# Optimization experiments

Hardware: AMD Instinct MI355X
Metric: run time of the kernel (lower is better)

## Reference

```python
import jax, jax.numpy as jnp
import numpy as np

H, DI, N, K, R, FF = 2048, 4096, 16, 4, 128, 5632
B, S = 2, 1024
EPS = 1e-6


def rmsnorm(x, w):
    v = jnp.mean(x * x, axis=-1, keepdims=True)
    return x * jax.lax.rsqrt(v + EPS) * w


def setup_inputs() -> dict:
    key = jax.random.key(0)
    ks = jax.random.split(key, 16)
    sc = 0.02
    inp = {
        "hidden_states": jax.random.normal(ks[0], (B, S, H), jnp.float32),
        "input_ln_w": jnp.ones((H,), jnp.float32),
        "w_in": jax.random.normal(ks[1], (2 * DI, H), jnp.float32) * sc,
        "conv_w": jax.random.normal(ks[2], (DI, 1, K), jnp.float32) * 0.3,
        "conv_b": jax.random.normal(ks[3], (DI,), jnp.float32) * sc,
        "w_x": jax.random.normal(ks[4], (R + 2 * N, DI), jnp.float32) * sc,
        "dt_ln_w": jnp.ones((R,), jnp.float32),
        "b_ln_w": jnp.ones((N,), jnp.float32),
        "c_ln_w": jnp.ones((N,), jnp.float32),
        "w_dt": jax.random.normal(ks[5], (DI, R), jnp.float32) * sc,
        "b_dt": jax.random.normal(ks[6], (DI,), jnp.float32) * sc - 4.0,
        "A_log": jnp.broadcast_to(jnp.log(jnp.arange(1, N + 1, dtype=jnp.float32)), (DI, N)),
        "D_skip": jnp.ones((DI,), jnp.float32),
        "w_out": jax.random.normal(ks[7], (H, DI), jnp.float32) * sc,
        "pre_ff_ln_w": jnp.ones((H,), jnp.float32),
        "w_gate": jax.random.normal(ks[8], (FF, H), jnp.float32) * sc,
        "w_up": jax.random.normal(ks[9], (FF, H), jnp.float32) * sc,
        "w_down": jax.random.normal(ks[10], (H, FF), jnp.float32) * sc,
    }
    return inp


def causal_conv1d(x, w, b):
    # x: [B,S,DI], w: [DI,1,K] depthwise, left-pad K-1 (causal)
    y = jax.lax.conv_general_dilated(
        x.transpose(0, 2, 1), w,
        window_strides=(1,), padding=[(K - 1, 0)],
        dimension_numbers=("NCH", "OIH", "NCH"),
        feature_group_count=DI)
    return (y + b[None, :, None]).transpose(0, 2, 1)


def selective_scan(u, A, Bm, Cm, Dp, dt):
    # u,dt: [B,S,DI]; A: [DI,N]; Bm,Cm: [B,S,N]
    def step(h, xs):
        dt_t, B_t, C_t, u_t = xs  # [B,DI],[B,N],[B,N],[B,DI]
        dA = jnp.exp(dt_t[:, :, None] * A)                      # [B,DI,N]
        dBu = dt_t[:, :, None] * B_t[:, None, :] * u_t[:, :, None]
        h = dA * h + dBu
        y = jnp.einsum("bdn,bn->bd", h, C_t)
        return h, y

    xs = (dt.transpose(1, 0, 2), Bm.transpose(1, 0, 2),
          Cm.transpose(1, 0, 2), u.transpose(1, 0, 2))
    h0 = jnp.zeros((u.shape[0], DI, N), u.dtype)
    _, ys = jax.lax.scan(step, h0, xs)
    return ys.transpose(1, 0, 2) + u * Dp  # [B,S,DI]


def reference(hidden_states, input_ln_w, w_in, conv_w, conv_b, w_x, dt_ln_w,
              b_ln_w, c_ln_w, w_dt, b_dt, A_log, D_skip, w_out, pre_ff_ln_w,
              w_gate, w_up, w_down):
    residual = hidden_states
    x = rmsnorm(hidden_states, input_ln_w)

    # --- Mamba mixer ---
    proj = x @ w_in.T                       # [B,S,2*DI]
    u, gate = jnp.split(proj, 2, axis=-1)
    u = jax.nn.silu(causal_conv1d(u, conv_w, conv_b))
    ssm_p = u @ w_x.T                       # [B,S,R+2N]
    t_r, Bm, Cm = jnp.split(ssm_p, [R, R + N], axis=-1)
    t_r = rmsnorm(t_r, dt_ln_w)
    Bm = rmsnorm(Bm, b_ln_w)
    Cm = rmsnorm(Cm, c_ln_w)
    dt = jax.nn.softplus(t_r @ w_dt.T + b_dt)  # [B,S,DI]
    A = -jnp.exp(A_log)
    y = selective_scan(u, A, Bm, Cm, D_skip, dt)
    y = y * jax.nn.silu(gate)
    mixer_out = y @ w_out.T                  # [B,S,H]

    hidden = residual + mixer_out
    residual = hidden
    h = rmsnorm(hidden, pre_ff_ln_w)
    ff = (jax.nn.silu(h @ w_gate.T) * (h @ w_up.T)) @ w_down.T
    return residual + ff
```

## Files before the change

### kernel.cpp

```cpp
#include <hip/hip_runtime.h>
#include <stdint.h>

#define H_   2048
#define DI_  4096
#define N_   16
#define K_   4
#define R_   128
#define FF_  5632
#define B_   2
#define S_   1024
#define MROWS (B_*S_)
#define PCH  16
#define CSTEPS (S_/PCH)

typedef float f32x4 __attribute__((ext_vector_type(4)));
typedef float f32x2 __attribute__((ext_vector_type(2)));
typedef __bf16 bf16x8 __attribute__((ext_vector_type(8)));

__device__ __forceinline__ unsigned short f2bf(float f) {
    union { float f; unsigned u; } v; v.f = f;
    unsigned r = v.u + 0x7fffu + ((v.u >> 16) & 1u);
    return (unsigned short)(r >> 16);
}

__device__ __forceinline__ float softplusf(float v) {
    return (v > 20.f) ? v : log1pf(__expf(v));
}

__device__ __forceinline__ void gload16(const void* g, void* lds) {
    __builtin_amdgcn_global_load_lds(
        (const __attribute__((address_space(1))) unsigned int*)(uintptr_t)g,
        (__attribute__((address_space(3))) unsigned int*)(unsigned int)(uintptr_t)lds,
        16, 0, 0);
}

__global__ __launch_bounds__(256, 2)
void gemm_bt(const unsigned short* __restrict__ A, const unsigned short* __restrict__ Bt,
             float* __restrict__ C, int M, int N, int K, int Kc)
{
    __shared__ __align__(16) unsigned short As[128 * 64];
    __shared__ __align__(16) unsigned short Bs[128 * 64];
    const int t = threadIdx.x;
    const int l = t & 63;
    const int wv = t >> 6;

    int nwg = gridDim.x * gridDim.y;
    int wg = blockIdx.y * gridDim.x + blockIdx.x;
    if ((nwg & 7) == 0) {
        int q = nwg >> 3;
        wg = (wg & 7) * q + (wg >> 3);
    }
    const int bx = wg % gridDim.x;
    const int by = wg / gridDim.x;
    const long m0 = (long)by * 128;
    const long n0 = (long)bx * 128;
    const int wm = (wv >> 1) * 64;
    const int wn = (wv & 1) * 64;
    const long kstart = (long)blockIdx.z * Kc;
    C += (long)blockIdx.z * M * (long)N;

    f32x4 acc[4][4] = {};

    const int tr = t >> 3;
    const int cs = (t & 7) ^ (tr & 7);
    const unsigned short* gA = A + (m0 + tr) * (long)K + kstart + cs * 8;
    const unsigned short* gB = Bt + (n0 + tr) * (long)K + kstart + cs * 8;
    const unsigned ldsbase = (unsigned)(t & 192) * 16;

    for (int kt = 0; kt < Kc; kt += 64) {
#pragma unroll
        for (int j = 0; j < 4; ++j) {
            gload16(gA + (long)j * 32 * K, (char*)As + j * 4096 + ldsbase);
            gload16(gB + (long)j * 32 * K, (char*)Bs + j * 4096 + ldsbase);
        }
        gA += 64; gB += 64;
        __syncthreads();
#pragma unroll
        for (int k0 = 0; k0 < 2; ++k0) {
            bf16x8 af[4], bfr[4];
#pragma unroll
            for (int i = 0; i < 4; ++i) {
                int rowa = wm + i * 16 + (l & 15);
                int ca = (k0 * 4 + (l >> 4)) ^ (rowa & 7);
                af[i] = *(const bf16x8*)(As + rowa * 64 + ca * 8);
                int rowb = wn + i * 16 + (l & 15);
                int cb = (k0 * 4 + (l >> 4)) ^ (rowb & 7);
                bfr[i] = *(const bf16x8*)(Bs + rowb * 64 + cb * 8);
            }
#pragma unroll
            for (int i = 0; i < 4; ++i)
#pragma unroll
                for (int jn = 0; jn < 4; ++jn)
                    acc[i][jn] = __builtin_amdgcn_mfma_f32_16x16x32_bf16(
                        af[i], bfr[jn], acc[i][jn], 0, 0, 0);
        }
        __syncthreads();
    }

    const int crow = (l >> 4) * 4;
    const int ccol = l & 15;
#pragma unroll
    for (int i = 0; i < 4; ++i) {
#pragma unroll
        for (int jn = 0; jn < 4; ++jn) {
            long row = m0 + wm + i * 16 + crow;
            long col = n0 + wn + jn * 16 + ccol;
            float* cp = C + row * (long)N + col;
#pragma unroll
            for (int q = 0; q < 4; ++q) cp[(long)q * N] = acc[i][jn][q];
        }
    }
}

__global__ __launch_bounds__(512, 1)
void gemm_bt256(const unsigned short* __restrict__ A, const unsigned short* __restrict__ Bt,
                float* __restrict__ C, int M, int N, int K, int Kc)
{
    __shared__ __align__(16) unsigned short As[2][256 * 64];
    __shared__ __align__(16) unsigned short Bs[2][256 * 64];
    const int t = threadIdx.x;
    const int l = t & 63;
    const int wv = t >> 6;
    const int wm = wv >> 2;
    const int wn = wv & 3;

    int nwg = gridDim.x * gridDim.y;
    int wg = blockIdx.y * gridDim.x + blockIdx.x;
    if ((nwg & 7) == 0) {
        int q = nwg >> 3;
        wg = (wg & 7) * q + (wg >> 3);
    }
    const int bx = wg % gridDim.x;
    const int by = wg / gridDim.x;
    const long m0 = (long)by * 256;
    const long n0 = (long)bx * 256;
    const long kstart = (long)blockIdx.z * Kc;
    C += (long)blockIdx.z * M * (long)N;

    f32x4 acc[8][4] = {};

    const int cs = (t & 7) ^ ((t >> 3) & 7);
    const unsigned short* gA = A + (m0 + (t >> 3)) * (long)K + kstart + cs * 8;
    const unsigned short* gB = Bt + (n0 + (t >> 3)) * (long)K + kstart + cs * 8;
    const int NT = Kc >> 6;

#pragma unroll
    for (int i = 0; i < 4; ++i)
        gload16(gA + (long)i * 64 * K, &As[0][t * 8 + i * 4096]);
#pragma unroll
    for (int i = 0; i < 4; ++i)
        gload16(gB + (long)i * 64 * K, &Bs[0][t * 8 + i * 4096]);

    for (int kt = 0; kt < NT; ++kt) {
        const int buf = kt & 1;
        const long koff = (long)((kt + 1 < NT) ? (kt + 1) : kt) * 64;
#pragma unroll
        for (int i = 0; i < 4; ++i)
            gload16(gA + koff + (long)i * 64 * K, &As[buf ^ 1][t * 8 + i * 4096]);
        asm volatile("s_waitcnt vmcnt(4)" ::: "memory");
        __builtin_amdgcn_sched_barrier(0);
        __builtin_amdgcn_s_barrier();
        __builtin_amdgcn_sched_barrier(0);
        {
            bf16x8 af[8], bfr[4];
#pragma unroll
            for (int nf = 0; nf < 4; ++nf) {
                int rowb = wn * 64 + nf * 16 + (l & 15);
                int cb = (l >> 4) ^ (rowb & 7);
                bfr[nf] = *(const bf16x8*)(&Bs[buf][rowb * 64 + cb * 8]);
            }
#pragma unroll
            for (int mf = 0; mf < 8; ++mf) {
                int rowa = wm * 128 + mf * 16 + (l & 15);
                int ca = (l >> 4) ^ (rowa & 7);
                af[mf] = *(const bf16x8*)(&As[buf][rowa * 64 + ca * 8]);
            }
            __builtin_amdgcn_s_setprio(1);
#pragma unroll
            for (int mf = 0; mf < 8; ++mf)
#pragma unroll
                for (int nf = 0; nf < 4; ++nf)
                    acc[mf][nf] = __builtin_amdgcn_mfma_f32_16x16x32_bf16(
                        af[mf], bfr[nf], acc[mf][nf], 0, 0, 0);
            __builtin_amdgcn_s_setprio(0);
        }
        __builtin_amdgcn_sched_barrier(0);
#pragma unroll
        for (int i = 0; i < 4; ++i)
            gload16(gB + koff + (long)i * 64 * K, &Bs[buf ^ 1][t * 8 + i * 4096]);
        {
            bf16x8 af[8], bfr[4];
#pragma unroll
            for (int nf = 0; nf < 4; ++nf) {
                int rowb = wn * 64 + nf * 16 + (l & 15);
                int cb = (4 + (l >> 4)) ^ (rowb & 7);
                bfr[nf] = *(const bf16x8*)(&Bs[buf][rowb * 64 + cb * 8]);
            }
#pragma unroll
            for (int mf = 0; mf < 8; ++mf) {
                int rowa = wm * 128 + mf * 16 + (l & 15);
                int ca = (4 + (l >> 4)) ^ (rowa & 7);
                af[mf] = *(const bf16x8*)(&As[buf][rowa * 64 + ca * 8]);
            }
            __builtin_amdgcn_s_setprio(1);
#pragma unroll
            for (int mf = 0; mf < 8; ++mf)
#pragma unroll
                for (int nf = 0; nf < 4; ++nf)
                    acc[mf][nf] = __builtin_amdgcn_mfma_f32_16x16x32_bf16(
                        af[mf], bfr[nf], acc[mf][nf], 0, 0, 0);
            __builtin_amdgcn_s_setprio(0);
        }
        __builtin_amdgcn_sched_barrier(0);
        __builtin_amdgcn_s_barrier();
        __builtin_amdgcn_sched_barrier(0);
    }

    const int crow = (l >> 4) * 4;
    const int ccol = l & 15;
#pragma unroll
    for (int mf = 0; mf < 8; ++mf) {
#pragma unroll
        for (int nf = 0; nf < 4; ++nf) {
            long row = m0 + wm * 128 + mf * 16 + crow;
            long col = n0 + wn * 64 + nf * 16 + ccol;
            float* cp = C + row * (long)N + col;
#pragma unroll
            for (int q = 0; q < 4; ++q) cp[(long)q * N] = acc[mf][nf][q];
        }
    }
}

__global__ __launch_bounds__(256)
void cvt_bf16(const float* __restrict__ x, unsigned short* __restrict__ y, long n)
{
    long i = ((long)blockIdx.x * 256 + threadIdx.x) * 4;
    if (i >= n) return;
    float4 v = *(const float4*)(x + i);
    ushort4 o;
    o.x = f2bf(v.x); o.y = f2bf(v.y); o.z = f2bf(v.z); o.w = f2bf(v.w);
    *(ushort4*)(y + i) = o;
}

__global__ __launch_bounds__(256)
void cvt_pad_wx(const float* __restrict__ x, unsigned short* __restrict__ y)
{
    long i = ((long)blockIdx.x * 256 + threadIdx.x) * 4;
    int row = (int)(i >> 12);
    ushort4 o;
    if (row < 160) {
        float4 v = *(const float4*)(x + i);
        o.x = f2bf(v.x); o.y = f2bf(v.y); o.z = f2bf(v.z); o.w = f2bf(v.w);
    } else { o.x = 0; o.y = 0; o.z = 0; o.w = 0; }
    *(ushort4*)(y + i) = o;
}

__global__ __launch_bounds__(256)
void rmsnorm_cast(const float* __restrict__ x, const float* __restrict__ w,
                  unsigned short* __restrict__ out)
{
    const long row = blockIdx.x;
    const float* xr = x + row * H_ + threadIdx.x * 8;
    float4 v0 = *(const float4*)xr;
    float4 v1 = *(const float4*)(xr + 4);
    float xv[8] = {v0.x, v0.y, v0.z, v0.w, v1.x, v1.y, v1.z, v1.w};
    float s = 0.f;
#pragma unroll
    for (int j = 0; j < 8; ++j) s += xv[j] * xv[j];
#pragma unroll
    for (int m = 32; m; m >>= 1) s += __shfl_xor(s, m);
    __shared__ float red[4];
    if ((threadIdx.x & 63) == 0) red[threadIdx.x >> 6] = s;
    __syncthreads();
    s = red[0] + red[1] + red[2] + red[3];
    float inv = rsqrtf(s * (1.f / H_) + 1e-6f);
    const float* wr = w + threadIdx.x * 8;
    unsigned short* op = out + row * H_ + threadIdx.x * 8;
    ushort4 o0, o1;
    o0.x = f2bf(xv[0] * inv * wr[0]); o0.y = f2bf(xv[1] * inv * wr[1]);
    o0.z = f2bf(xv[2] * inv * wr[2]); o0.w = f2bf(xv[3] * inv * wr[3]);
    o1.x = f2bf(xv[4] * inv * wr[4]); o1.y = f2bf(xv[5] * inv * wr[5]);
    o1.z = f2bf(xv[6] * inv * wr[6]); o1.w = f2bf(xv[7] * inv * wr[7]);
    *(ushort4*)op = o0;
    *(ushort4*)(op + 4) = o1;
}

__global__ __launch_bounds__(256)
void add_rmsnorm(const float* __restrict__ a, const float* __restrict__ mx,
                 const float* __restrict__ w, float* __restrict__ hid,
                 unsigned short* __restrict__ hb)
{
    const long row = blockIdx.x;
    const long off = row * H_ + threadIdx.x * 8;
    float xv[8];
    {
        float4 a0 = *(const float4*)(a + off);
        float4 a1 = *(const float4*)(a + off + 4);
        xv[0] = a0.x; xv[1] = a0.y; xv[2] = a0.z; xv[3] = a0.w;
        xv[4] = a1.x; xv[5] = a1.y; xv[6] = a1.z; xv[7] = a1.w;
    }
#pragma unroll
    for (int z = 0; z < 4; ++z) {
        const float* mz = mx + (long)z * MROWS * H_ + off;
        float4 b0 = *(const float4*)mz;
        float4 b1 = *(const float4*)(mz + 4);
        xv[0] += b0.x; xv[1] += b0.y; xv[2] += b0.z; xv[3] += b0.w;
        xv[4] += b1.x; xv[5] += b1.y; xv[6] += b1.z; xv[7] += b1.w;
    }
    float s = 0.f;
#pragma unroll
    for (int j = 0; j < 8; ++j) s += xv[j] * xv[j];
#pragma unroll
    for (int m = 32; m; m >>= 1) s += __shfl_xor(s, m);
    __shared__ float red[4];
    if ((threadIdx.x & 63) == 0) red[threadIdx.x >> 6] = s;
    __syncthreads();
    s = red[0] + red[1] + red[2] + red[3];
    float inv = rsqrtf(s * (1.f / H_) + 1e-6f);
    float4 h0, h1;
    h0.x = xv[0]; h0.y = xv[1]; h0.z = xv[2]; h0.w = xv[3];
    h1.x = xv[4]; h1.y = xv[5]; h1.z = xv[6]; h1.w = xv[7];
    *(float4*)(hid + off) = h0;
    *(float4*)(hid + off + 4) = h1;
    const float* wr = w + threadIdx.x * 8;
    ushort4 o0, o1;
    o0.x = f2bf(xv[0] * inv * wr[0]); o0.y = f2bf(xv[1] * inv * wr[1]);
    o0.z = f2bf(xv[2] * inv * wr[2]); o0.w = f2bf(xv[3] * inv * wr[3]);
    o1.x = f2bf(xv[4] * inv * wr[4]); o1.y = f2bf(xv[5] * inv * wr[5]);
    o1.z = f2bf(xv[6] * inv * wr[6]); o1.w = f2bf(xv[7] * inv * wr[7]);
    *(ushort4*)(hb + off) = o0;
    *(ushort4*)(hb + off + 4) = o1;
}

__global__ __launch_bounds__(256)
void conv_silu(const float* __restrict__ proj, const float* __restrict__ cw,
               const float* __restrict__ cb, float* __restrict__ uf,
               unsigned short* __restrict__ ub)
{
    long i = (long)blockIdx.x * 256 + threadIdx.x;
    int d = (int)(i & (DI_ - 1));
    long sd = i >> 12;
    int s = (int)(sd & (S_ - 1));
    long rb = sd * (2 * DI_) + d;
    float w0 = cw[d * 4], w1 = cw[d * 4 + 1], w2 = cw[d * 4 + 2], w3 = cw[d * 4 + 3];
    float acc = cb[d] + w3 * proj[rb];
    if (s >= 1) acc += w2 * proj[rb - 2 * DI_];
    if (s >= 2) acc += w1 * proj[rb - 4 * DI_];
    if (s >= 3) acc += w0 * proj[rb - 6 * DI_];
    float r = acc / (1.f + __expf(-acc));
    uf[i] = r;
    ub[i] = f2bf(r);
}

__global__ __launch_bounds__(256)
void ssm_norms(const float* __restrict__ ssmp, const float* __restrict__ wdt,
               const float* __restrict__ wb, const float* __restrict__ wc,
               unsigned short* __restrict__ trb, float* __restrict__ Bm,
               float* __restrict__ Cm)
{
    const long row = (long)blockIdx.x * 4 + (threadIdx.x >> 6);
    const int l = threadIdx.x & 63;
    float x0 = 0.f, x1 = 0.f, xb = 0.f, xc = 0.f;
#pragma unroll
    for (int z = 0; z < 8; ++z) {
        const float* rp = ssmp + (long)z * (MROWS * 256) + row * 256;
        x0 += rp[l];
        x1 += rp[64 + l];
        xb += rp[128 + (l & 15)];
        xc += rp[144 + (l & 15)];
    }
    float s = x0 * x0 + x1 * x1;
#pragma unroll
    for (int m = 32; m; m >>= 1) s += __shfl_xor(s, m);
    float inv = rsqrtf(s * (1.f / R_) + 1e-6f);
    trb[row * R_ + l] = f2bf(x0 * inv * wdt[l]);
    trb[row * R_ + 64 + l] = f2bf(x1 * inv * wdt[64 + l]);

    float sb = xb * xb, sc = xc * xc;
#pragma unroll
    for (int m = 8; m; m >>= 1) { sb += __shfl_xor(sb, m); sc += __shfl_xor(sc, m); }
    float invb = rsqrtf(sb * (1.f / N_) + 1e-6f);
    float invc = rsqrtf(sc * (1.f / N_) + 1e-6f);
    if (l < 16) {
        Bm[row * N_ + l] = xb * invb * wb[l];
        Cm[row * N_ + l] = xc * invc * wc[l];
    }
}


__global__ __launch_bounds__(256)
void scan_partA(const float* __restrict__ uf, const float* __restrict__ dtraw,
                const float* __restrict__ bdt, const float* __restrict__ Bm,
                const float* __restrict__ A_log,
                float* __restrict__ TRH, float* __restrict__ TRS)
{
    __shared__ __align__(16) float UD[4][16][16][2];
    __shared__ __align__(16) float BBs[4][16][16];

    const int w = threadIdx.x >> 6;
    const int l = threadIdx.x & 63;
    const int ch = l & 15, sgx = l >> 4;
    const int task = blockIdx.x * 4 + w;
    const int dchunk = task >> 4;
    const int p = task & 15;
    const int gch0 = dchunk * 16;
    const int batch = gch0 >> 12;
    const int d0 = gch0 & (DI_ - 1);
    const int d = d0 + ch;
    const long bS = (long)batch * S_;
    const int t0 = p * CSTEPS;

    f32x4 Av;
    {
        f32x4 al = *(const f32x4*)&A_log[(long)d * N_ + sgx * 4];
        Av[0] = -__expf(al[0]); Av[1] = -__expf(al[1]);
        Av[2] = -__expf(al[2]); Av[3] = -__expf(al[3]);
    }
    const int sA = l >> 2;
    const int c4 = (l & 3) * 4;
    const f32x4 bias4 = *(const f32x4*)&bdt[d0 + c4];

    f32x4 u4, t4, b4;
    {
        long row = bS + t0 + sA;
        u4 = *(const f32x4*)&uf[row * DI_ + d0 + c4];
        f32x4 tr = *(const f32x4*)&dtraw[row * DI_ + d0 + c4];
#pragma unroll
        for (int j = 0; j < 4; ++j) t4[j] = softplusf(tr[j] + bias4[j]);
        b4 = *(const f32x4*)&Bm[(bS + t0) * N_ + l * 4];
    }

    float h0 = 0.f, h1 = 0.f, h2 = 0.f, h3 = 0.f, sdt = 0.f;

    for (int ck = 0; ck < 4; ++ck) {
#pragma unroll
        for (int j = 0; j < 4; ++j) {
            f32x2 wv; wv[0] = t4[j]; wv[1] = u4[j] * t4[j];
            *(f32x2*)&UD[w][sA][c4 + j][0] = wv;
        }
        *(f32x4*)((float*)&BBs[w][0][0] + l * 4) = b4;
        if (ck + 1 < 4) {
            long row = bS + t0 + (ck + 1) * 16 + sA;
            u4 = *(const f32x4*)&uf[row * DI_ + d0 + c4];
            f32x4 tr = *(const f32x4*)&dtraw[row * DI_ + d0 + c4];
#pragma unroll
            for (int j = 0; j < 4; ++j) t4[j] = softplusf(tr[j] + bias4[j]);
            b4 = *(const f32x4*)&Bm[(bS + t0 + (ck + 1) * 16) * N_ + l * 4];
        }
#pragma unroll
        for (int s = 0; s < 16; ++s) {
            f32x2 dd = *(const f32x2*)&UD[w][s][ch][0];
            f32x4 B4 = *(const f32x4*)&BBs[w][s][sgx * 4];
            float cdt = dd[0], dtu = dd[1];
            h0 = __expf(cdt * Av[0]) * h0 + dtu * B4[0];
            h1 = __expf(cdt * Av[1]) * h1 + dtu * B4[1];
            h2 = __expf(cdt * Av[2]) * h2 + dtu * B4[2];
            h3 = __expf(cdt * Av[3]) * h3 + dtu * B4[3];
            sdt += cdt;
        }
    }
    f32x4 hv; hv[0] = h0; hv[1] = h1; hv[2] = h2; hv[3] = h3;
    *(f32x4*)&TRH[((long)(gch0 + ch)) * (PCH * 16) + p * 16 + sgx * 4] = hv;
    if (l < 16) TRS[(gch0 + l) * PCH + p] = sdt;
}

__global__ __launch_bounds__(256)
void scan_combine(const float* __restrict__ A_log, const float* __restrict__ TRS,
                  float* __restrict__ TRH)
{
    const int tid = blockIdx.x * 256 + threadIdx.x;
    const int gch = tid >> 4, n = tid & 15;
    const int d = gch & (DI_ - 1);
    const float Av = -__expf(A_log[(long)d * N_ + n]);
    const float* sp = TRS + (long)gch * PCH;
    float* hp = TRH + (long)gch * (PCH * 16) + n;
    float h = 0.f;
#pragma unroll
    for (int p = 0; p < PCH; ++p) {
        float hl = hp[p * 16];
        float e = __expf(Av * sp[p]);
        hp[p * 16] = h;
        h = hl + e * h;
    }
}

__global__ __launch_bounds__(256)
void scan_partC(const float* __restrict__ uf, const float* __restrict__ dtraw,
                const float* __restrict__ bdt, const float* __restrict__ Bm,
                const float* __restrict__ Cm, const float* __restrict__ A_log,
                const float* __restrict__ Dskip, const float* __restrict__ proj,
                const float* __restrict__ TRH, unsigned short* __restrict__ yb)
{
    __shared__ __align__(16) float UDG[4][16][16][4];
    __shared__ __align__(16) float BBs[4][16][16];
    __shared__ __align__(16) float CCs[4][16][16];

    const int w = threadIdx.x >> 6;
    const int l = threadIdx.x & 63;
    const int ch = l & 15, sgx = l >> 4;
    const int task = blockIdx.x * 4 + w;
    const int dchunk = task >> 4;
    const int p = task & 15;
    const int gch0 = dchunk * 16;
    const int batch = gch0 >> 12;
    const int d0 = gch0 & (DI_ - 1);
    const int d = d0 + ch;
    const long bS = (long)batch * S_;
    const int t0 = p * CSTEPS;

    f32x4 Av;
    {
        f32x4 al = *(const f32x4*)&A_log[(long)d * N_ + sgx * 4];
        Av[0] = -__expf(al[0]); Av[1] = -__expf(al[1]);
        Av[2] = -__expf(al[2]); Av[3] = -__expf(al[3]);
    }
    const float Dv = Dskip[d];

    f32x4 hv = *(const f32x4*)&TRH[((long)(gch0 + ch)) * (PCH * 16) + p * 16 + sgx * 4];
    float h0 = hv[0], h1 = hv[1], h2 = hv[2], h3 = hv[3];

    const int sA = l >> 2;
    const int c4 = (l & 3) * 4;
    const f32x4 bias4 = *(const f32x4*)&bdt[d0 + c4];

    f32x4 u4, t4, g4, b4, c4v;
    {
        long row = bS + t0 + sA;
        u4 = *(const f32x4*)&uf[row * DI_ + d0 + c4];
        f32x4 tr = *(const f32x4*)&dtraw[row * DI_ + d0 + c4];
#pragma unroll
        for (int j = 0; j < 4; ++j) t4[j] = softplusf(tr[j] + bias4[j]);
        g4 = *(const f32x4*)&proj[row * (2L * DI_) + DI_ + d0 + c4];
        b4 = *(const f32x4*)&Bm[(bS + t0) * N_ + l * 4];
        c4v = *(const f32x4*)&Cm[(bS + t0) * N_ + l * 4];
    }

    for (int ck = 0; ck < 4; ++ck) {
#pragma unroll
        for (int j = 0; j < 4; ++j) {
            f32x4 wv;
            wv[0] = u4[j]; wv[1] = t4[j]; wv[2] = g4[j]; wv[3] = u4[j] * t4[j];
            *(f32x4*)&UDG[w][sA][c4 + j][0] = wv;
        }
        *(f32x4*)((float*)&BBs[w][0][0] + l * 4) = b4;
        *(f32x4*)((float*)&CCs[w][0][0] + l * 4) = c4v;
        if (ck + 1 < 4) {
            long row = bS + t0 + (ck + 1) * 16 + sA;
            u4 = *(const f32x4*)&uf[row * DI_ + d0 + c4];
            f32x4 tr = *(const f32x4*)&dtraw[row * DI_ + d0 + c4];
#pragma unroll
            for (int j = 0; j < 4; ++j) t4[j] = softplusf(tr[j] + bias4[j]);
            g4 = *(const f32x4*)&proj[row * (2L * DI_) + DI_ + d0 + c4];
            b4 = *(const f32x4*)&Bm[(bS + t0 + (ck + 1) * 16) * N_ + l * 4];
            c4v = *(const f32x4*)&Cm[(bS + t0 + (ck + 1) * 16) * N_ + l * 4];
        }
#pragma unroll
        for (int s = 0; s < 16; ++s) {
            f32x4 udg = *(const f32x4*)&UDG[w][s][ch][0];
            f32x4 B4 = *(const f32x4*)&BBs[w][s][sgx * 4];
            f32x4 C4 = *(const f32x4*)&CCs[w][s][sgx * 4];
            float cdt = udg[1], dtu = udg[3];
            h0 = __expf(cdt * Av[0]) * h0 + dtu * B4[0];
            h1 = __expf(cdt * Av[1]) * h1 + dtu * B4[1];
            h2 = __expf(cdt * Av[2]) * h2 + dtu * B4[2];
            h3 = __expf(cdt * Av[3]) * h3 + dtu * B4[3];
            float pr = (h0 * C4[0] + h1 * C4[1]) + (h2 * C4[2] + h3 * C4[3]);
            pr += __shfl_xor(pr, 16);
            pr += __shfl_xor(pr, 32);
            if (l < 16) {
                float y = pr + udg[0] * Dv;
                float cg = udg[2];
                float sl = cg / (1.f + __expf(-cg));
                yb[(bS + t0 + ck * 16 + s) * DI_ + d] = f2bf(y * sl);
            }
        }
    }
}

__global__ __launch_bounds__(256)
void silu_mul(const float* __restrict__ g, const float* __restrict__ u,
              unsigned short* __restrict__ out, long n)
{
    long i = ((long)blockIdx.x * 256 + threadIdx.x) * 4;
    if (i >= n) return;
    float4 gv = *(const float4*)(g + i);
    float4 uv = *(const float4*)(u + i);
    ushort4 o;
    o.x = f2bf(gv.x / (1.f + __expf(-gv.x)) * uv.x);
    o.y = f2bf(gv.y / (1.f + __expf(-gv.y)) * uv.y);
    o.z = f2bf(gv.z / (1.f + __expf(-gv.z)) * uv.z);
    o.w = f2bf(gv.w / (1.f + __expf(-gv.w)) * uv.w);
    *(ushort4*)(out + i) = o;
}

__global__ __launch_bounds__(256)
void final_add(const float* __restrict__ a, const float* __restrict__ b,
               float* __restrict__ y, long n)
{
    long i = ((long)blockIdx.x * 256 + threadIdx.x) * 4;
    if (i >= n) return;
    float4 av = *(const float4*)(a + i);
    float4 o = av;
#pragma unroll
    for (int z = 0; z < 4; ++z) {
        float4 bv = *(const float4*)(b + (long)z * MROWS * H_ + i);
        o.x += bv.x; o.y += bv.y; o.z += bv.z; o.w += bv.w;
    }
    *(float4*)(y + i) = o;
}

extern "C" void kernel_launch(void* const* d_in, const int* in_sizes, int n_in,
                              void* d_out, int out_size, void* d_ws, size_t ws_size,
                              hipStream_t stream)
{
    const float* hs     = (const float*)d_in[0];
    const float* ln_in  = (const float*)d_in[1];
    const float* w_in   = (const float*)d_in[2];
    const float* conv_w = (const float*)d_in[3];
    const float* conv_b = (const float*)d_in[4];
    const float* w_x    = (const float*)d_in[5];
    const float* dt_ln  = (const float*)d_in[6];
    const float* b_ln   = (const float*)d_in[7];
    const float* c_ln   = (const float*)d_in[8];
    const float* w_dt   = (const float*)d_in[9];
    const float* b_dt   = (const float*)d_in[10];
    const float* A_log  = (const float*)d_in[11];
    const float* Dskip  = (const float*)d_in[12];
    const float* w_out  = (const float*)d_in[13];
    const float* ln_ff  = (const float*)d_in[14];
    const float* w_gate = (const float*)d_in[15];
    const float* w_up   = (const float*)d_in[16];
    const float* w_down = (const float*)d_in[17];
    float* out = (float*)d_out;
    char* ws = (char*)d_ws;

    unsigned short* WB    = (unsigned short*)(ws + 0L);
    unsigned short* XB    = (unsigned short*)(ws + 33554432L);
    float*          PROJ  = (float*)(ws + 41943040L);
    float*          MIX   = (float*)(ws + 41943040L);
    float*          GF    = (float*)(ws + 41943040L);
    float*          FFT   = (float*)(ws + 41943040L);
    float*          UF    = (float*)(ws + 109051904L);
    unsigned short* FFACT = (unsigned short*)(ws + 109051904L);
    unsigned short* UB    = (unsigned short*)(ws + 142606336L);
    float*          HID   = (float*)(ws + 142606336L);
    unsigned short* TRB   = (unsigned short*)(ws + 159383552L);
    float*          BM    = (float*)(ws + 159907840L);
    float*          CM    = (float*)(ws + 160038912L);
    float*          TRS   = (float*)(ws + 160169984L);
    float*          SSMP  = (float*)(ws + 160694272L);
    float*          DTRAW = (float*)(ws + 160694272L);
    float*          TRH   = (float*)(ws + 194248704L);
    float*          UPF   = (float*)(ws + 194248704L);
    unsigned short* YB    = (unsigned short*)(ws + 227803136L);
    unsigned short* HB    = XB;

    auto gemm = [&](const unsigned short* A, const unsigned short* Bt, float* C,
                    int M, int N, int K, int kch) {
        dim3 g(N / 128, M / 128, kch);
        gemm_bt<<<g, 256, 0, stream>>>(A, Bt, C, M, N, K, K / kch);
    };
    auto gemm256 = [&](const unsigned short* A, const unsigned short* Bt, float* C,
                       int M, int N, int K, int kch) {
        dim3 g(N / 256, M / 256, kch);
        gemm_bt256<<<g, 512, 0, stream>>>(A, Bt, C, M, N, K, K / kch);
    };
    auto cvt = [&](const float* x, unsigned short* y, long n) {
        cvt_bf16<<<(int)((n / 4 + 255) / 256), 256, 0, stream>>>(x, y, n);
    };

    cvt(w_in, WB, (long)2 * DI_ * H_);
    rmsnorm_cast<<<MROWS, 256, 0, stream>>>(hs, ln_in, XB);
    gemm256(XB, WB, PROJ, MROWS, 2 * DI_, H_, 1);
    conv_silu<<<(MROWS * DI_) / 256, 256, 0, stream>>>(PROJ, conv_w, conv_b, UF, UB);
    cvt_pad_wx<<<(256 * DI_ / 4) / 256, 256, 0, stream>>>(w_x, WB);
    gemm(UB, WB, SSMP, MROWS, 256, DI_, 8);
    ssm_norms<<<MROWS / 4, 256, 0, stream>>>(SSMP, dt_ln, b_ln, c_ln, TRB, BM, CM);
    cvt(w_dt, WB, (long)DI_ * R_);
    gemm(TRB, WB, DTRAW, MROWS, DI_, R_, 1);
    scan_partA<<<(B_ * DI_ / 16) * PCH / 4, 256, 0, stream>>>(UF, DTRAW, b_dt, BM,
                                                              A_log, TRH, TRS);
    scan_combine<<<(B_ * DI_ * N_) / 256, 256, 0, stream>>>(A_log, TRS, TRH);
    scan_partC<<<(B_ * DI_ / 16) * PCH / 4, 256, 0, stream>>>(UF, DTRAW, b_dt, BM, CM,
                                                              A_log, Dskip, PROJ, TRH, YB);
    cvt(w_out, WB, (long)H_ * DI_);
    gemm256(YB, WB, MIX, MROWS, H_, DI_, 4);
    add_rmsnorm<<<MROWS, 256, 0, stream>>>(hs, MIX, ln_ff, HID, HB);
    cvt(w_gate, WB, (long)FF_ * H_);
    gemm256(HB, WB, GF, MROWS, FF_, H_, 1);
    cvt(w_up, WB, (long)FF_ * H_);
    gemm256(HB, WB, UPF, MROWS, FF_, H_, 1);
    silu_mul<<<(int)(((long)MROWS * FF_ / 4 + 255) / 256), 256, 0, stream>>>(
        GF, UPF, FFACT, (long)MROWS * FF_);
    cvt(w_down, WB, (long)H_ * FF_);
    gemm256(FFACT, WB, FFT, MROWS, H_, FF_, 4);
    final_add<<<(int)(((long)MROWS * H_ / 4 + 255) / 256), 256, 0, stream>>>(
        HID, FFT, out, (long)MROWS * H_);
}
```

Before: 599.7 us.

## Restructure selective scan to one channel per lane with all states in registers

Scan kernels now give each lane one channel and hold all 16 state values in registers. This removes the LDS staging and the cross-lane shuffle reduction for y. The sequence is split into 32 chunks instead of 16, for more parallelism with shorter chunks. Exp, log and reciprocal now use native exp2, log2 and rcp builtins, and the workspace offsets are moved to fit the larger TRH/TRS buffers. The costs are higher register pressure, scalar per-lane loads of B and C that every lane repeats, and slightly lower precision in softplus.

```diff
diff --git a/kernel.cpp b/kernel.cpp
--- a/kernel.cpp
+++ b/kernel.cpp
@@ -10,12 +10,15 @@
 #define B_   2
 #define S_   1024
 #define MROWS (B_*S_)
-#define PCH  16
+#define PCH  32
 #define CSTEPS (S_/PCH)
 
 typedef float f32x4 __attribute__((ext_vector_type(4)));
 typedef float f32x2 __attribute__((ext_vector_type(2)));
 typedef __bf16 bf16x8 __attribute__((ext_vector_type(8)));
+
+#define LOG2E 1.4426950408889634f
+#define LN2   0.6931471805599453f
 
 __device__ __forceinline__ unsigned short f2bf(float f) {
     union { float f; unsigned u; } v; v.f = f;
@@ -23,8 +26,11 @@
     return (unsigned short)(r >> 16);
 }
 
-__device__ __forceinline__ float softplusf(float v) {
-    return (v > 20.f) ? v : log1pf(__expf(v));
+__device__ __forceinline__ float fexp2(float x) { return __builtin_amdgcn_exp2f(x); }
+__device__ __forceinline__ float flog2(float x) { return __builtin_amdgcn_logf(x); }
+
+__device__ __forceinline__ float softplus2(float v) {
+    return (v > 20.f) ? v : LN2 * flog2(1.f + fexp2(v * LOG2E));
 }
 
 __device__ __forceinline__ void gload16(const void* g, void* lds) {
@@ -394,74 +400,64 @@
                 const float* __restrict__ A_log,
                 float* __restrict__ TRH, float* __restrict__ TRS)
 {
-    __shared__ __align__(16) float UD[4][16][16][2];
-    __shared__ __align__(16) float BBs[4][16][16];
-
-    const int w = threadIdx.x >> 6;
+    const int w = __builtin_amdgcn_readfirstlane(threadIdx.x >> 6);
     const int l = threadIdx.x & 63;
-    const int ch = l & 15, sgx = l >> 4;
     const int task = blockIdx.x * 4 + w;
-    const int dchunk = task >> 4;
-    const int p = task & 15;
-    const int gch0 = dchunk * 16;
+    const int dchunk = task >> 5;
+    const int p = task & 31;
+    const int gch0 = dchunk * 64;
     const int batch = gch0 >> 12;
     const int d0 = gch0 & (DI_ - 1);
-    const int d = d0 + ch;
+    const int d = d0 + l;
     const long bS = (long)batch * S_;
     const int t0 = p * CSTEPS;
 
-    f32x4 Av;
+    float Av2[16];
+#pragma unroll
+    for (int n = 0; n < 16; ++n)
+        Av2[n] = -fexp2(A_log[(long)d * N_ + n] * LOG2E) * LOG2E;
+    const float bias = bdt[d];
+
+    float h[16];
+#pragma unroll
+    for (int n = 0; n < 16; ++n) h[n] = 0.f;
+    float sdt = 0.f;
+
+    float uN = uf[(bS + t0) * DI_ + d];
+    float tN = dtraw[(bS + t0) * DI_ + d];
+    float BN[16];
     {
-        f32x4 al = *(const f32x4*)&A_log[(long)d * N_ + sgx * 4];
-        Av[0] = -__expf(al[0]); Av[1] = -__expf(al[1]);
-        Av[2] = -__expf(al[2]); Av[3] = -__expf(al[3]);
-    }
-    const int sA = l >> 2;
-    const int c4 = (l & 3) * 4;
-    const f32x4 bias4 = *(const f32x4*)&bdt[d0 + c4];
-
-    f32x4 u4, t4, b4;
-    {
-        long row = bS + t0 + sA;
-        u4 = *(const f32x4*)&uf[row * DI_ + d0 + c4];
-        f32x4 tr = *(const f32x4*)&dtraw[row * DI_ + d0 + c4];
-#pragma unroll
-        for (int j = 0; j < 4; ++j) t4[j] = softplusf(tr[j] + bias4[j]);
-        b4 = *(const f32x4*)&Bm[(bS + t0) * N_ + l * 4];
-    }
-
-    float h0 = 0.f, h1 = 0.f, h2 = 0.f, h3 = 0.f, sdt = 0.f;
-
-    for (int ck = 0; ck < 4; ++ck) {
-#pragma unroll
-        for (int j = 0; j < 4; ++j) {
-            f32x2 wv; wv[0] = t4[j]; wv[1] = u4[j] * t4[j];
-            *(f32x2*)&UD[w][sA][c4 + j][0] = wv;
-        }
-        *(f32x4*)((float*)&BBs[w][0][0] + l * 4) = b4;
-        if (ck + 1 < 4) {
-            long row = bS + t0 + (ck + 1) * 16 + sA;
-            u4 = *(const f32x4*)&uf[row * DI_ + d0 + c4];
-            f32x4 tr = *(const f32x4*)&dtraw[row * DI_ + d0 + c4];
-#pragma unroll
-            for (int j = 0; j < 4; ++j) t4[j] = softplusf(tr[j] + bias4[j]);
-            b4 = *(const f32x4*)&Bm[(bS + t0 + (ck + 1) * 16) * N_ + l * 4];
-        }
-#pragma unroll
-        for (int s = 0; s < 16; ++s) {
-            f32x2 dd = *(const f32x2*)&UD[w][s][ch][0];
-            f32x4 B4 = *(const f32x4*)&BBs[w][s][sgx * 4];
-            float cdt = dd[0], dtu = dd[1];
-            h0 = __expf(cdt * Av[0]) * h0 + dtu * B4[0];
-            h1 = __expf(cdt * Av[1]) * h1 + dtu * B4[1];
-            h2 = __expf(cdt * Av[2]) * h2 + dtu * B4[2];
-            h3 = __expf(cdt * Av[3]) * h3 + dtu * B4[3];
-            sdt += cdt;
-        }
-    }
-    f32x4 hv; hv[0] = h0; hv[1] = h1; hv[2] = h2; hv[3] = h3;
-    *(f32x4*)&TRH[((long)(gch0 + ch)) * (PCH * 16) + p * 16 + sgx * 4] = hv;
-    if (l < 16) TRS[(gch0 + l) * PCH + p] = sdt;
+        const float* Bp = Bm + (bS + t0) * N_;
+#pragma unroll
+        for (int n = 0; n < 16; ++n) BN[n] = Bp[n];
+    }
+
+    for (int s = 0; s < CSTEPS; ++s) {
+        float uC = uN, tC = tN;
+        float BC[16];
+#pragma unroll
+        for (int n = 0; n < 16; ++n) BC[n] = BN[n];
+        if (s + 1 < CSTEPS) {
+            long r2 = bS + t0 + s + 1;
+            uN = uf[r2 * DI_ + d];
+            tN = dtraw[r2 * DI_ + d];
+            const float* Bp = Bm + r2 * N_;
+#pragma unroll
+            for (int n = 0; n < 16; ++n) BN[n] = Bp[n];
+        }
+        float dt = softplus2(tC + bias);
+        float dtu = dt * uC;
+        sdt += dt;
+#pragma unroll
+        for (int n = 0; n < 16; ++n) {
+            float e = fexp2(dt * Av2[n]);
+            h[n] = fmaf(e, h[n], dtu * BC[n]);
+        }
+    }
+    float* hp = &TRH[(long)(gch0 + l) * (PCH * 16) + p * 16];
+#pragma unroll
+    for (int n = 0; n < 16; ++n) hp[n] = h[n];
+    TRS[(long)(gch0 + l) * PCH + p] = sdt;
 }
 
 __global__ __launch_bounds__(256)
@@ -491,89 +487,70 @@
                 const float* __restrict__ Dskip, const float* __restrict__ proj,
                 const float* __restrict__ TRH, unsigned short* __restrict__ yb)
 {
-    __shared__ __align__(16) float UDG[4][16][16][4];
-    __shared__ __align__(16) float BBs[4][16][16];
-    __shared__ __align__(16) float CCs[4][16][16];
-
-    const int w = threadIdx.x >> 6;
+    const int w = __builtin_amdgcn_readfirstlane(threadIdx.x >> 6);
     const int l = threadIdx.x & 63;
-    const int ch = l & 15, sgx = l >> 4;
     const int task = blockIdx.x * 4 + w;
-    const int dchunk = task >> 4;
-    const int p = task & 15;
-    const int gch0 = dchunk * 16;
+    const int dchunk = task >> 5;
+    const int p = task & 31;
+    const int gch0 = dchunk * 64;
     const int batch = gch0 >> 12;
     const int d0 = gch0 & (DI_ - 1);
-    const int d = d0 + ch;
+    const int d = d0 + l;
     const long bS = (long)batch * S_;
     const int t0 = p * CSTEPS;
 
-    f32x4 Av;
+    float Av2[16];
+#pragma unroll
+    for (int n = 0; n < 16; ++n)
+        Av2[n] = -fexp2(A_log[(long)d * N_ + n] * LOG2E) * LOG2E;
+    const float bias = bdt[d];
+    const float Dv = Dskip[d];
+
+    float h[16];
     {
-        f32x4 al = *(const f32x4*)&A_log[(long)d * N_ + sgx * 4];
-        Av[0] = -__expf(al[0]); Av[1] = -__expf(al[1]);
-        Av[2] = -__expf(al[2]); Av[3] = -__expf(al[3]);
-    }
-    const float Dv = Dskip[d];
-
-    f32x4 hv = *(const f32x4*)&TRH[((long)(gch0 + ch)) * (PCH * 16) + p * 16 + sgx * 4];
-    float h0 = hv[0], h1 = hv[1], h2 = hv[2], h3 = hv[3];
-
-    const int sA = l >> 2;
-    const int c4 = (l & 3) * 4;
-    const f32x4 bias4 = *(const f32x4*)&bdt[d0 + c4];
-
-    f32x4 u4, t4, g4, b4, c4v;
+        const float* hp = &TRH[(long)(gch0 + l) * (PCH * 16) + p * 16];
+#pragma unroll
+        for (int n = 0; n < 16; ++n) h[n] = hp[n];
+    }
+
+    float uN = uf[(bS + t0) * DI_ + d];
+    float tN = dtraw[(bS + t0) * DI_ + d];
+    float gN = proj[(bS + t0) * (2L * DI_) + DI_ + d];
+    float BN[16], CN[16];
     {
-        long row = bS + t0 + sA;
-        u4 = *(const f32x4*)&uf[row * DI_ + d0 + c4];
-        f32x4 tr = *(const f32x4*)&dtraw[row * DI_ + d0 + c4];
-#pragma unroll
-        for (int j = 0; j < 4; ++j) t4[j] = softplusf(tr[j] + bias4[j]);
-        g4 = *(const f32x4*)&proj[row * (2L * DI_) + DI_ + d0 + c4];
-        b4 = *(const f32x4*)&Bm[(bS + t0) * N_ + l * 4];
-        c4v = *(const f32x4*)&Cm[(bS + t0) * N_ + l * 4];
-    }
-
-    for (int ck = 0; ck < 4; ++ck) {
-#pragma unroll
-        for (int j = 0; j < 4; ++j) {
-            f32x4 wv;
-            wv[0] = u4[j]; wv[1] = t4[j]; wv[2] = g4[j]; wv[3] = u4[j] * t4[j];
-            *(f32x4*)&UDG[w][sA][c4 + j][0] = wv;
-        }
-        *(f32x4*)((float*)&BBs[w][0][0] + l * 4) = b4;
-        *(f32x4*)((float*)&CCs[w][0][0] + l * 4) = c4v;
-        if (ck + 1 < 4) {
-            long row = bS + t0 + (ck + 1) * 16 + sA;
-            u4 = *(const f32x4*)&uf[row * DI_ + d0 + c4];
-            f32x4 tr = *(const f32x4*)&dtraw[row * DI_ + d0 + c4];
-#pragma unroll
-            for (int j = 0; j < 4; ++j) t4[j] = softplusf(tr[j] + bias4[j]);
-            g4 = *(const f32x4*)&proj[row * (2L * DI_) + DI_ + d0 + c4];
-            b4 = *(const f32x4*)&Bm[(bS + t0 + (ck + 1) * 16) * N_ + l * 4];
-            c4v = *(const f32x4*)&Cm[(bS + t0 + (ck + 1) * 16) * N_ + l * 4];
-        }
-#pragma unroll
-        for (int s = 0; s < 16; ++s) {
-            f32x4 udg = *(const f32x4*)&UDG[w][s][ch][0];
-            f32x4 B4 = *(const f32x4*)&BBs[w][s][sgx * 4];
-            f32x4 C4 = *(const f32x4*)&CCs[w][s][sgx * 4];
-            float cdt = udg[1], dtu = udg[3];
-            h0 = __expf(cdt * Av[0]) * h0 + dtu * B4[0];
-            h1 = __expf(cdt * Av[1]) * h1 + dtu * B4[1];
-            h2 = __expf(cdt * Av[2]) * h2 + dtu * B4[2];
-            h3 = __expf(cdt * Av[3]) * h3 + dtu * B4[3];
-            float pr = (h0 * C4[0] + h1 * C4[1]) + (h2 * C4[2] + h3 * C4[3]);
-            pr += __shfl_xor(pr, 16);
-            pr += __shfl_xor(pr, 32);
-            if (l < 16) {
-                float y = pr + udg[0] * Dv;
-                float cg = udg[2];
-                float sl = cg / (1.f + __expf(-cg));
-                yb[(bS + t0 + ck * 16 + s) * DI_ + d] = f2bf(y * sl);
-            }
-        }
+        const float* Bp = Bm + (bS + t0) * N_;
+        const float* Cp = Cm + (bS + t0) * N_;
+#pragma unroll
+        for (int n = 0; n < 16; ++n) { BN[n] = Bp[n]; CN[n] = Cp[n]; }
+    }
+
+    for (int s = 0; s < CSTEPS; ++s) {
+        float uC = uN, tC = tN, gC = gN;
+        float BC[16], CC_[16];
+#pragma unroll
+        for (int n = 0; n < 16; ++n) { BC[n] = BN[n]; CC_[n] = CN[n]; }
+        if (s + 1 < CSTEPS) {
+            long r2 = bS + t0 + s + 1;
+            uN = uf[r2 * DI_ + d];
+            tN = dtraw[r2 * DI_ + d];
+            gN = proj[r2 * (2L * DI_) + DI_ + d];
+            const float* Bp = Bm + r2 * N_;
+            const float* Cp = Cm + r2 * N_;
+#pragma unroll
+            for (int n = 0; n < 16; ++n) { BN[n] = Bp[n]; CN[n] = Cp[n]; }
+        }
+        float dt = softplus2(tC + bias);
+        float dtu = dt * uC;
+        float y = uC * Dv;
+#pragma unroll
+        for (int n = 0; n < 16; ++n) {
+            float e = fexp2(dt * Av2[n]);
+            h[n] = fmaf(e, h[n], dtu * BC[n]);
+            y = fmaf(h[n], CC_[n], y);
+        }
+        float eg = fexp2(-gC * LOG2E);
+        float sl = gC * __builtin_amdgcn_rcpf(1.f + eg);
+        yb[(bS + t0 + s) * DI_ + d] = f2bf(y * sl);
     }
 }
 
@@ -648,10 +625,10 @@
     float*          BM    = (float*)(ws + 159907840L);
     float*          CM    = (float*)(ws + 160038912L);
     float*          TRS   = (float*)(ws + 160169984L);
-    float*          SSMP  = (float*)(ws + 160694272L);
-    float*          DTRAW = (float*)(ws + 160694272L);
-    float*          TRH   = (float*)(ws + 194248704L);
-    float*          UPF   = (float*)(ws + 194248704L);
+    float*          SSMP  = (float*)(ws + 161218560L);
+    float*          DTRAW = (float*)(ws + 161218560L);
+    float*          TRH   = (float*)(ws + 194772992L);
+    float*          UPF   = (float*)(ws + 161218560L);
     unsigned short* YB    = (unsigned short*)(ws + 227803136L);
     unsigned short* HB    = XB;
 
@@ -678,10 +655,10 @@
     ssm_norms<<<MROWS / 4, 256, 0, stream>>>(SSMP, dt_ln, b_ln, c_ln, TRB, BM, CM);
     cvt(w_dt, WB, (long)DI_ * R_);
     gemm(TRB, WB, DTRAW, MROWS, DI_, R_, 1);
-    scan_partA<<<(B_ * DI_ / 16) * PCH / 4, 256, 0, stream>>>(UF, DTRAW, b_dt, BM,
+    scan_partA<<<(B_ * DI_ / 64) * PCH / 4, 256, 0, stream>>>(UF, DTRAW, b_dt, BM,
                                                               A_log, TRH, TRS);
     scan_combine<<<(B_ * DI_ * N_) / 256, 256, 0, stream>>>(A_log, TRS, TRH);
-    scan_partC<<<(B_ * DI_ / 16) * PCH / 4, 256, 0, stream>>>(UF, DTRAW, b_dt, BM, CM,
+    scan_partC<<<(B_ * DI_ / 64) * PCH / 4, 256, 0, stream>>>(UF, DTRAW, b_dt, BM, CM,
                                                               A_log, Dskip, PROJ, TRH, YB);
     cvt(w_out, WB, (long)H_ * DI_);
     gemm256(YB, WB, MIX, MROWS, H_, DI_, 4);
```

New measurement: 538.9 us. 10.1% less time.
